# Optimization experiments

Measured on AMD Instinct MI355X. Metric: run time of the kernel, lower is better.

## Reference

```python
import jax, jax.numpy as jnp
import numpy as np

GMAX = 1.0   # args.gmax
GMIN = 0.01  # args.gmin
EPS = 0.1    # args.e_train


def setup_inputs() -> dict:
    key = jax.random.key(0)
    k1, k2, k3, k4 = jax.random.split(key, 4)
    N, B, NIN, NOUT, E = 8, 32, 128, 128, 1024
    # analog signals live in [0, 1]
    a_previous = jax.random.uniform(k1, (N, B, NIN, E), dtype=jnp.float32)
    # conductance params (clamped to [-gmax, gmax] in forward)
    theta = jax.random.uniform(k2, (NIN + 2, NOUT), dtype=jnp.float32) * 2.0 - 1.0
    # per-replica multiplicative noise seed in [0, 1); forward maps to 1 +- eps
    noise = jax.random.uniform(k3, (N, NIN + 2, NOUT), dtype=jnp.float32)
    # printed-tanh activation params eta = [offset, scale, shift, slope]
    eta = jnp.array([0.0, 1.0, 0.0, 1.0], dtype=jnp.float32) + 0.1 * jax.random.normal(k4, (4,), dtype=jnp.float32)
    return {"a_previous": a_previous, "theta": theta, "noise": noise, "eta": eta}


def reference(a_previous, theta, noise, eta):
    sg = jax.lax.stop_gradient
    # theta property: clamp + gmin pruning with straight-through estimator
    t = jnp.clip(theta, -GMAX, GMAX)
    t = jnp.where(jnp.abs(t) < GMIN, 0.0, t)
    theta_eff = sg(t) + theta - sg(theta)
    # theta_noisy: replicate over N with multiplicative uniform noise in [1-eps, 1+eps]
    theta_noisy = theta_eff[None, :, :] * ((noise * 2.0 - 1.0) * EPS + 1.0)  # [N, M, O], M = n_in+2
    # W: abs-normalized conductances per output column group
    abs_tn = jnp.abs(theta_noisy)
    W = abs_tn / (jnp.sum(abs_tn, axis=1, keepdims=True) + 1e-10)
    # sign masks (constants w.r.t. grad: values fully overwritten in torch)
    pos = sg((theta_noisy >= 0.0).astype(theta_noisy.dtype))
    neg = 1.0 - pos
    # a: [N, B, n_in, E] -> [N, B, E, n_in]; append ones and zeros columns
    a_r = jnp.transpose(a_previous, (0, 1, 3, 2))
    ones = jnp.ones(a_r.shape[:3] + (1,), a_r.dtype)
    zeros = jnp.zeros_like(ones)
    a_ext = jnp.concatenate([a_r, ones, zeros], axis=3)  # [N, B, E, M]
    # INV: unipolar complement; zero the last (zeros) column after inversion
    a_neg = (1.0 - a_ext).at[..., -1].set(0.0)
    # split-sign MAC: z [N, B, E, n_out]
    z = (jnp.einsum('nbem,nmo->nbeo', a_ext, W * pos)
         + jnp.einsum('nbem,nmo->nbeo', a_neg, W * neg))
    # printed tanh activation
    act = eta[0] + eta[1] * jnp.tanh((z - eta[2]) * eta[3])
    # back to [N, B, n_out, E]
    return jnp.transpose(act, (0, 1, 3, 2))
```

## Files before the change

kernel.cpp:

```cpp
#include <hip/hip_runtime.h>
#include <stdint.h>

#define N_REP 8
#define BATCH 32
#define NIN   128
#define NOUT  128
#define EDIM  1024
#define MDIM  130
#define ETILE 128

typedef __attribute__((ext_vector_type(8))) short short8;
typedef __attribute__((ext_vector_type(4))) float f32x4;

__device__ __forceinline__ unsigned short f2bf(float f) {
    union { float f; uint32_t u; } v;
    v.f = f;
    uint32_t u = v.u;
    uint32_t r = u + 0x7fffu + ((u >> 16) & 1u);
    return (unsigned short)(r >> 16);
}

__global__ void prep_kernel(const float* __restrict__ theta,
                            const float* __restrict__ noise,
                            unsigned short* __restrict__ Sg,
                            float* __restrict__ biasg) {
    const int n = blockIdx.x;
    const int o = threadIdx.x;
    const float* nptr = noise + (size_t)n * MDIM * NOUT + o;
    float sum = 0.f;
    for (int m = 0; m < MDIM; ++m) {
        float t = theta[m * NOUT + o];
        t = fminf(fmaxf(t, -1.f), 1.f);
        if (fabsf(t) < 0.01f) t = 0.f;
        float tn = t * fmaf(nptr[m * NOUT], 0.2f, 0.9f);
        sum += fabsf(tn);
    }
    const float inv = 1.f / (sum + 1e-10f);
    float bias = 0.f;
    unsigned short* srow = Sg + ((size_t)n * NOUT + o) * NIN;
    for (int m = 0; m < MDIM; ++m) {
        float t = theta[m * NOUT + o];
        t = fminf(fmaxf(t, -1.f), 1.f);
        if (fabsf(t) < 0.01f) t = 0.f;
        float tn = t * fmaf(nptr[m * NOUT], 0.2f, 0.9f);
        float w = fabsf(tn) * inv;
        if (m < NIN) {
            srow[m] = f2bf(tn >= 0.f ? w : -w);
            if (tn < 0.f) bias += w;
        } else if (m == NIN) {
            if (tn >= 0.f) bias += w;
        }
    }
    biasg[n * NOUT + o] = bias;
}

__global__ __launch_bounds__(256, 2)
void gemm_kernel(const float* __restrict__ a,
                 const unsigned short* __restrict__ Sg,
                 const float* __restrict__ biasg,
                 const float* __restrict__ eta,
                 float* __restrict__ out) {
    __shared__ float Alds[NIN * ETILE];
    const int bid = blockIdx.x;
    const int et  = bid & 7;
    const int nb  = bid >> 3;
    const int n   = nb >> 5;
    const int tid = threadIdx.x;

    {
        const float* abase = a + (size_t)nb * (NIN * EDIM) + et * ETILE;
        const int e4 = (tid & 31) << 2;
        const int m0 = tid >> 5;
#pragma unroll
        for (int it = 0; it < 16; ++it) {
            const int m = m0 + (it << 3);
            const float4 v = *(const float4*)(abase + (size_t)m * EDIM + e4);
            const int x = ((m >> 3) & 1) << 4;
            *(float4*)&Alds[m * ETILE + (e4 ^ x)] = v;
        }
    }
    __syncthreads();

    const int lane = tid & 63;
    const int w = tid >> 6;
    const int r = lane & 15;
    const int q = lane >> 4;
    const int o_base = (w & 1) << 6;
    const int e_base = (w >> 1) << 6;

    short8 sf[4][4];
#pragma unroll
    for (int fo = 0; fo < 4; ++fo) {
        const int o = o_base + (fo << 4) + r;
        const unsigned short* sp = Sg + ((size_t)(n * NOUT + o) << 7) + (q << 3);
#pragma unroll
        for (int ks = 0; ks < 4; ++ks)
            sf[fo][ks] = *(const short8*)(sp + (ks << 5));
    }

    f32x4 acc[4][4];
#pragma unroll
    for (int fo = 0; fo < 4; ++fo)
#pragma unroll
        for (int fe = 0; fe < 4; ++fe)
            acc[fo][fe] = (f32x4){0.f, 0.f, 0.f, 0.f};

    const int xq = (q & 1) << 4;
#pragma unroll
    for (int ks = 0; ks < 4; ++ks) {
        short8 af[4];
#pragma unroll
        for (int fe = 0; fe < 4; ++fe) {
            const int e = (e_base + (fe << 4) + r) ^ xq;
            const int mrow = (ks << 5) + (q << 3);
            short8 t;
#pragma unroll
            for (int j = 0; j < 8; ++j)
                t[j] = (short)f2bf(Alds[(mrow + j) * ETILE + e]);
            af[fe] = t;
        }
#pragma unroll
        for (int fo = 0; fo < 4; ++fo)
#pragma unroll
            for (int fe = 0; fe < 4; ++fe)
                acc[fo][fe] = __builtin_amdgcn_mfma_f32_16x16x32_bf16(
                    sf[fo][ks], af[fe], acc[fo][fe], 0, 0, 0);
    }

    const float e0 = eta[0], e1 = eta[1], e2 = eta[2], e3 = eta[3];
    float* obase = out + (size_t)nb * (NOUT * EDIM) + et * ETILE;
#pragma unroll
    for (int fo = 0; fo < 4; ++fo) {
#pragma unroll
        for (int i = 0; i < 4; ++i) {
            const int o = o_base + (fo << 4) + (q << 2) + i;
            const float bias = biasg[n * NOUT + o];
            float* orow = obase + (size_t)o * EDIM;
#pragma unroll
            for (int fe = 0; fe < 4; ++fe) {
                const float z = acc[fo][fe][i] + bias;
                const float y = (z - e2) * e3;
                const float ex = __expf(2.f * y);
                const float th = 1.f - 2.f * __builtin_amdgcn_rcpf(ex + 1.f);
                orow[e_base + (fe << 4) + r] = fmaf(e1, th, e0);
            }
        }
    }
}

extern "C" void kernel_launch(void* const* d_in, const int* in_sizes, int n_in,
                              void* d_out, int out_size, void* d_ws, size_t ws_size,
                              hipStream_t stream) {
    const float* a     = (const float*)d_in[0];
    const float* theta = (const float*)d_in[1];
    const float* noise = (const float*)d_in[2];
    const float* eta   = (const float*)d_in[3];
    float* out = (float*)d_out;

    unsigned short* Sg = (unsigned short*)d_ws;
    float* biasg = (float*)((char*)d_ws + (size_t)N_REP * NOUT * NIN * sizeof(unsigned short));

    prep_kernel<<<N_REP, NOUT, 0, stream>>>(theta, noise, Sg, biasg);
    gemm_kernel<<<N_REP * BATCH * (EDIM / ETILE), 256, 0, stream>>>(a, Sg, biasg, eta, out);
}
```

Baseline: 288.6 us.

## Stage A as packed bf16 pairs in LDS, parallelize prep, raise occupancy

The gemm kernel now converts activations to bf16 while loading them from global memory, storing pairs of rows packed into 32-bit words in a padded LDS tile. This halves LDS use (about 33KB instead of 64KB) and removes the per-element conversion from the MFMA operand gather. Weight fragments are loaded per k-step instead of all up front, and launch bounds ask for 4 blocks per CU. Separately, the prep kernel now uses one wave per (replica, output) pair with shuffle reductions instead of a serial loop per thread, and bias is loaded as float4. The cost is extra global loads of weight fragments inside the k loop, plus possible LDS bank conflicts from the new padded layout.

```diff
diff --git a/kernel.cpp b/kernel.cpp
--- a/kernel.cpp
+++ b/kernel.cpp
@@ -1,4 +1,5 @@
 #include <hip/hip_runtime.h>
+#include <hip/hip_bf16.h>
 #include <stdint.h>
 
 #define N_REP 8
@@ -8,6 +9,7 @@
 #define EDIM  1024
 #define MDIM  130
 #define ETILE 128
+#define SE    130
 
 typedef __attribute__((ext_vector_type(8))) short short8;
 typedef __attribute__((ext_vector_type(4))) float f32x4;
@@ -20,47 +22,58 @@
     return (unsigned short)(r >> 16);
 }
 
-__global__ void prep_kernel(const float* __restrict__ theta,
-                            const float* __restrict__ noise,
-                            unsigned short* __restrict__ Sg,
-                            float* __restrict__ biasg) {
-    const int n = blockIdx.x;
-    const int o = threadIdx.x;
-    const float* nptr = noise + (size_t)n * MDIM * NOUT + o;
-    float sum = 0.f;
-    for (int m = 0; m < MDIM; ++m) {
+__device__ __forceinline__ uint32_t pk2bf(float lo, float hi) {
+    __hip_bfloat162 h = __float22bfloat162_rn(make_float2(lo, hi));
+    uint32_t d;
+    __builtin_memcpy(&d, &h, 4);
+    return d;
+}
+
+__global__ __launch_bounds__(64)
+void prep_kernel(const float* __restrict__ theta,
+                 const float* __restrict__ noise,
+                 unsigned short* __restrict__ Sg,
+                 float* __restrict__ biasg) {
+    const int n = blockIdx.x >> 7;
+    const int o = blockIdx.x & 127;
+    const int lane = threadIdx.x;
+
+    const float* nb = noise + (size_t)n * MDIM * NOUT + o;
+    auto tn_at = [&](int m) -> float {
         float t = theta[m * NOUT + o];
         t = fminf(fmaxf(t, -1.f), 1.f);
         if (fabsf(t) < 0.01f) t = 0.f;
-        float tn = t * fmaf(nptr[m * NOUT], 0.2f, 0.9f);
-        sum += fabsf(tn);
-    }
-    const float inv = 1.f / (sum + 1e-10f);
-    float bias = 0.f;
+        return t * fmaf(nb[m * NOUT], 0.2f, 0.9f);
+    };
+
+    const float t0 = tn_at(lane);
+    const float t1 = tn_at(lane + 64);
+    const float t2 = (lane < 2) ? tn_at(128 + lane) : 0.f;
+
+    float s = fabsf(t0) + fabsf(t1) + fabsf(t2);
+#pragma unroll
+    for (int d = 1; d < 64; d <<= 1) s += __shfl_xor(s, d, 64);
+    const float inv = 1.f / (s + 1e-10f);
+
+    const float w0 = fabsf(t0) * inv, w1 = fabsf(t1) * inv;
     unsigned short* srow = Sg + ((size_t)n * NOUT + o) * NIN;
-    for (int m = 0; m < MDIM; ++m) {
-        float t = theta[m * NOUT + o];
-        t = fminf(fmaxf(t, -1.f), 1.f);
-        if (fabsf(t) < 0.01f) t = 0.f;
-        float tn = t * fmaf(nptr[m * NOUT], 0.2f, 0.9f);
-        float w = fabsf(tn) * inv;
-        if (m < NIN) {
-            srow[m] = f2bf(tn >= 0.f ? w : -w);
-            if (tn < 0.f) bias += w;
-        } else if (m == NIN) {
-            if (tn >= 0.f) bias += w;
-        }
-    }
-    biasg[n * NOUT + o] = bias;
+    srow[lane]      = f2bf(t0 >= 0.f ? w0 : -w0);
+    srow[lane + 64] = f2bf(t1 >= 0.f ? w1 : -w1);
+
+    float b = (t0 < 0.f ? w0 : 0.f) + (t1 < 0.f ? w1 : 0.f);
+    if (lane == 0 && t2 >= 0.f) b += fabsf(t2) * inv;
+#pragma unroll
+    for (int d = 1; d < 64; d <<= 1) b += __shfl_xor(b, d, 64);
+    if (lane == 0) biasg[n * NOUT + o] = b;
 }
 
-__global__ __launch_bounds__(256, 2)
+__global__ __launch_bounds__(256, 4)
 void gemm_kernel(const float* __restrict__ a,
                  const unsigned short* __restrict__ Sg,
                  const float* __restrict__ biasg,
                  const float* __restrict__ eta,
                  float* __restrict__ out) {
-    __shared__ float Alds[NIN * ETILE];
+    __shared__ uint32_t Alds[64 * SE];
     const int bid = blockIdx.x;
     const int et  = bid & 7;
     const int nb  = bid >> 3;
@@ -69,14 +82,20 @@
 
     {
         const float* abase = a + (size_t)nb * (NIN * EDIM) + et * ETILE;
-        const int e4 = (tid & 31) << 2;
-        const int m0 = tid >> 5;
+        const int e4  = (tid & 31) << 2;
+        const int mp0 = tid >> 5;
 #pragma unroll
-        for (int it = 0; it < 16; ++it) {
-            const int m = m0 + (it << 3);
-            const float4 v = *(const float4*)(abase + (size_t)m * EDIM + e4);
-            const int x = ((m >> 3) & 1) << 4;
-            *(float4*)&Alds[m * ETILE + (e4 ^ x)] = v;
+        for (int it = 0; it < 8; ++it) {
+            const int mp = mp0 + (it << 3);
+            const float4 va = *(const float4*)(abase + (size_t)(2 * mp) * EDIM + e4);
+            const float4 vb = *(const float4*)(abase + (size_t)(2 * mp + 1) * EDIM + e4);
+            uint2 d0, d1;
+            d0.x = pk2bf(va.x, vb.x);
+            d0.y = pk2bf(va.y, vb.y);
+            d1.x = pk2bf(va.z, vb.z);
+            d1.y = pk2bf(va.w, vb.w);
+            *(uint2*)&Alds[mp * SE + e4]     = d0;
+            *(uint2*)&Alds[mp * SE + e4 + 2] = d1;
         }
     }
     __syncthreads();
@@ -88,16 +107,6 @@
     const int o_base = (w & 1) << 6;
     const int e_base = (w >> 1) << 6;
 
-    short8 sf[4][4];
-#pragma unroll
-    for (int fo = 0; fo < 4; ++fo) {
-        const int o = o_base + (fo << 4) + r;
-        const unsigned short* sp = Sg + ((size_t)(n * NOUT + o) << 7) + (q << 3);
-#pragma unroll
-        for (int ks = 0; ks < 4; ++ks)
-            sf[fo][ks] = *(const short8*)(sp + (ks << 5));
-    }
-
     f32x4 acc[4][4];
 #pragma unroll
     for (int fo = 0; fo < 4; ++fo)
@@ -105,40 +114,46 @@
         for (int fe = 0; fe < 4; ++fe)
             acc[fo][fe] = (f32x4){0.f, 0.f, 0.f, 0.f};
 
-    const int xq = (q & 1) << 4;
 #pragma unroll
     for (int ks = 0; ks < 4; ++ks) {
+        short8 sf[4];
+#pragma unroll
+        for (int fo = 0; fo < 4; ++fo) {
+            const int o = o_base + (fo << 4) + r;
+            sf[fo] = *(const short8*)(Sg + ((size_t)(n * NOUT + o) << 7) + (ks << 5) + (q << 3));
+        }
         short8 af[4];
+        const int mpb = (ks << 4) + (q << 2);
 #pragma unroll
         for (int fe = 0; fe < 4; ++fe) {
-            const int e = (e_base + (fe << 4) + r) ^ xq;
-            const int mrow = (ks << 5) + (q << 3);
-            short8 t;
+            const int e = e_base + (fe << 4) + r;
+            uint32_t d[4];
 #pragma unroll
-            for (int j = 0; j < 8; ++j)
-                t[j] = (short)f2bf(Alds[(mrow + j) * ETILE + e]);
-            af[fe] = t;
+            for (int jj = 0; jj < 4; ++jj)
+                d[jj] = Alds[(mpb + jj) * SE + e];
+            __builtin_memcpy(&af[fe], d, 16);
         }
 #pragma unroll
         for (int fo = 0; fo < 4; ++fo)
 #pragma unroll
             for (int fe = 0; fe < 4; ++fe)
                 acc[fo][fe] = __builtin_amdgcn_mfma_f32_16x16x32_bf16(
-                    sf[fo][ks], af[fe], acc[fo][fe], 0, 0, 0);
+                    sf[fo], af[fe], acc[fo][fe], 0, 0, 0);
     }
 
     const float e0 = eta[0], e1 = eta[1], e2 = eta[2], e3 = eta[3];
     float* obase = out + (size_t)nb * (NOUT * EDIM) + et * ETILE;
 #pragma unroll
     for (int fo = 0; fo < 4; ++fo) {
+        const int orow0 = o_base + (fo << 4) + (q << 2);
+        const float4 bias4 = *(const float4*)(biasg + n * NOUT + orow0);
+        const float bv[4] = {bias4.x, bias4.y, bias4.z, bias4.w};
 #pragma unroll
         for (int i = 0; i < 4; ++i) {
-            const int o = o_base + (fo << 4) + (q << 2) + i;
-            const float bias = biasg[n * NOUT + o];
-            float* orow = obase + (size_t)o * EDIM;
+            float* orow = obase + (size_t)(orow0 + i) * EDIM;
 #pragma unroll
             for (int fe = 0; fe < 4; ++fe) {
-                const float z = acc[fo][fe][i] + bias;
+                const float z = acc[fo][fe][i] + bv[i];
                 const float y = (z - e2) * e3;
                 const float ex = __expf(2.f * y);
                 const float th = 1.f - 2.f * __builtin_amdgcn_rcpf(ex + 1.f);
@@ -160,6 +175,6 @@
     unsigned short* Sg = (unsigned short*)d_ws;
     float* biasg = (float*)((char*)d_ws + (size_t)N_REP * NOUT * NIN * sizeof(unsigned short));
 
-    prep_kernel<<<N_REP, NOUT, 0, stream>>>(theta, noise, Sg, biasg);
+    prep_kernel<<<N_REP * NOUT, 64, 0, stream>>>(theta, noise, Sg, biasg);
     gemm_kernel<<<N_REP * BATCH * (EDIM / ETILE), 256, 0, stream>>>(a, Sg, biasg, eta, out);
 }
```

Measured after the change: 254.6 us. 11.8% less time.
